# Performance work log

Measured on AMD Instinct MI355X. Metric: run time of the kernel, lower is better.

Reference implementation:

```python
import jax, jax.numpy as jnp
import numpy as np

B, S, D, H = 2, 2048, 1024, 16
DH = D // H  # 64


def setup_inputs() -> dict:
    key = jax.random.key(0)
    ks = jax.random.split(key, 12)
    scale = 0.02
    q = jax.random.normal(ks[0], (B, S, D), dtype=jnp.float32)
    k = jax.random.normal(ks[1], (B, S, D), dtype=jnp.float32)
    v = jax.random.normal(ks[2], (B, S, D), dtype=jnp.float32)
    # CTRL-style causal mask: 1.0 above the diagonal (positions to mask), 0.0 elsewhere
    mask = jnp.triu(jnp.ones((S, S), dtype=jnp.float32), k=1)
    Wq = jax.random.normal(ks[3], (D, D), dtype=jnp.float32) * scale
    bq = jnp.zeros((D,), dtype=jnp.float32)
    Wk = jax.random.normal(ks[4], (D, D), dtype=jnp.float32) * scale
    bk = jnp.zeros((D,), dtype=jnp.float32)
    Wv = jax.random.normal(ks[5], (D, D), dtype=jnp.float32) * scale
    bv = jnp.zeros((D,), dtype=jnp.float32)
    Wo = jax.random.normal(ks[6], (D, D), dtype=jnp.float32) * scale
    bo = jnp.zeros((D,), dtype=jnp.float32)
    return {"q": q, "k": k, "v": v, "mask": mask,
            "Wq": Wq, "bq": bq, "Wk": Wk, "bk": bk,
            "Wv": Wv, "bv": bv, "Wo": Wo, "bo": bo}


def _split_heads(x):
    # [B, S, D] -> [B, H, S, DH]
    b, s, _ = x.shape
    return x.reshape(b, s, H, DH).transpose(0, 2, 1, 3)


def reference(q, k, v, mask, Wq, bq, Wk, bk, Wv, bv, Wo, bo):
    # QKV projections
    qh = _split_heads(q @ Wq + bq)  # [B, H, S, DH]
    kh = _split_heads(k @ Wk + bk)
    vh = _split_heads(v @ Wv + bv)
    # scaled dot-product attention with CTRL mask convention (mask * -1e4 added)
    scores = jnp.einsum('bhqd,bhkd->bhqk', qh, kh) / jnp.sqrt(jnp.float32(DH))
    scores = scores + mask * -10000.0  # mask broadcasts [S,S] -> [B,H,S,S]
    weights = jax.nn.softmax(scores, axis=-1)
    ctx = jnp.einsum('bhqk,bhkd->bhqd', weights, vh)  # [B, H, S, DH]
    ctx = ctx.transpose(0, 2, 1, 3).reshape(q.shape[0], -1, D)  # [B, S, D]
    return ctx @ Wo + bo
```

## Files before the change

kernel.cpp:

```cpp
#include <hip/hip_runtime.h>
#include <stdint.h>

typedef unsigned short u16;
typedef __attribute__((ext_vector_type(8))) short bf16x8;
typedef __attribute__((ext_vector_type(4))) float f32x4;
typedef __attribute__((ext_vector_type(4))) unsigned short u16x4;

#define C_SCALE 0.1803368801111204f
#define C_MASK  -14426.950408889634f

__device__ __forceinline__ float bf2f(u16 x) {
  union { uint32_t u; float f; } v; v.u = ((uint32_t)x) << 16; return v.f;
}
__device__ __forceinline__ u16 f2bf(float f) {
  union { float f; uint32_t u; } v; v.f = f;
  return (u16)((v.u + 0x7FFFu + ((v.u >> 16) & 1u)) >> 16);
}

__device__ __forceinline__ void load_lds16(const void* g, void* l) {
  __builtin_amdgcn_global_load_lds(
      (const __attribute__((address_space(1))) uint32_t*)g,
      (__attribute__((address_space(3))) uint32_t*)l, 16, 0, 0);
}

__device__ __forceinline__ uint32_t pack_trunc(uint32_t f_even, uint32_t f_odd) {
  return __builtin_amdgcn_perm(f_odd, f_even, 0x07060302u);
}

__device__ __forceinline__ bool detect_bf16(const u16* __restrict__ q) {
  int lane = threadIdx.x & 63;
  u16 w = q[lane * 4];
  int e = (w >> 7) & 0xFF;
  unsigned long long b = __ballot(e >= 96 && e <= 159);
  return __popcll(b) >= 48;
}

__global__ __launch_bounds__(256) void transpose_all(const u16* __restrict__ W0,
                                                     const u16* __restrict__ W1,
                                                     const u16* __restrict__ W2,
                                                     const u16* __restrict__ W3,
                                                     u16* __restrict__ WTb,
                                                     const u16* __restrict__ qprobe) {
  constexpr int D = 1024;
  __shared__ u16 tile[64][72];
  const int z = blockIdx.z;
  const u16* W = z == 0 ? W0 : (z == 1 ? W1 : (z == 2 ? W2 : W3));
  u16* WT = WTb + (size_t)z * D * D;
  const bool isbf = detect_bf16(qprobe);
  const int x0 = blockIdx.x * 64, y0 = blockIdx.y * 64;
  const int t = threadIdx.x;
  const int r = t >> 3;
  const int c8 = (t & 7) << 3;
#pragma unroll
  for (int hh = 0; hh < 2; ++hh) {
    int row = r + hh * 32;
    if (isbf) {
      *(uint4*)&tile[row][c8] = *(const uint4*)&W[(size_t)(y0 + row) * D + x0 + c8];
    } else {
      const float* Wf = (const float*)W;
      float4 f0 = *(const float4*)&Wf[(size_t)(y0 + row) * D + x0 + c8];
      float4 f1 = *(const float4*)&Wf[(size_t)(y0 + row) * D + x0 + c8 + 4];
      u16 tmp[8] = {f2bf(f0.x), f2bf(f0.y), f2bf(f0.z), f2bf(f0.w),
                    f2bf(f1.x), f2bf(f1.y), f2bf(f1.z), f2bf(f1.w)};
      *(uint4*)&tile[row][c8] = *(uint4*)tmp;
    }
  }
  __syncthreads();
#pragma unroll
  for (int hh = 0; hh < 2; ++hh) {
    int row = r + hh * 32;
    u16 tmp[8];
#pragma unroll
    for (int i = 0; i < 8; ++i) tmp[i] = tile[c8 + i][row];
    *(uint4*)&WT[(size_t)(x0 + row) * D + y0 + c8] = *(uint4*)tmp;
  }
}


__device__ __forceinline__ void stage_tile32(const u16* __restrict__ src, int row0,
                                             int k0, u16* dst, int wave, int lane) {
  constexpr int K = 1024;
#pragma unroll
  for (int p = 0; p < 2; ++p) {
    int seg = wave * 2 + p;
    int r = seg * 16 + (lane >> 2);
    int c = lane & 3;
    int cg = c ^ ((r >> 1) & 3);
    load_lds16(&src[(size_t)(row0 + r) * K + k0 + cg * 8], dst + seg * 512);
  }
}

#define FRAG_READS(Ab, Bb)                                                    \
  _Pragma("unroll") for (int i = 0; i < 4; ++i) {                             \
    int r = wm + 16 * i + lr;                                                 \
    af[i] = *(const bf16x8*)&(Ab)[r * 32 + ((quad ^ ((r >> 1) & 3)) * 8)];    \
  }                                                                           \
  _Pragma("unroll") for (int jj = 0; jj < 4; ++jj) {                          \
    int r = wn + 16 * jj + lr;                                                \
    bff[jj] = *(const bf16x8*)&(Bb)[r * 32 + ((quad ^ ((r >> 1) & 3)) * 8)];  \
  }

#define MFMA16()                                                              \
  _Pragma("unroll") for (int i = 0; i < 4; ++i)                               \
  _Pragma("unroll") for (int jj = 0; jj < 4; ++jj)                            \
      acc[i][jj] = __builtin_amdgcn_mfma_f32_16x16x32_bf16(af[i], bff[jj],    \
                                                           acc[i][jj], 0, 0, 0);

__device__ __forceinline__ void kloop2_dma(const u16* __restrict__ A,
                                           const u16* __restrict__ BT,
                                           int m0, int n0, u16* As, u16* Bs,
                                           int wave, int lane, f32x4 (&acc)[4][4]) {
  const int quad = lane >> 4, lr = lane & 15;
  const int wm = (wave & 1) * 64, wn = (wave >> 1) * 64;
  auto stage = [&](int t, int buf) {
    stage_tile32(A, m0, t * 32, As + buf * 4096, wave, lane);
    stage_tile32(BT, n0, t * 32, Bs + buf * 4096, wave, lane);
  };
  stage(0, 0);
  __syncthreads();
#pragma unroll 1
  for (int j = 0; j < 16; ++j) {
    const int t0 = 2 * j;
    {
      stage(t0 + 1, 1);
      bf16x8 af[4], bff[4];
      const u16 *Ab = As, *Bb = Bs;
      FRAG_READS(Ab, Bb)
      MFMA16()
      __syncthreads();
    }
    {
      if (t0 + 2 < 32) stage(t0 + 2, 0);
      bf16x8 af[4], bff[4];
      const u16 *Ab = As + 4096, *Bb = Bs + 4096;
      FRAG_READS(Ab, Bb)
      MFMA16()
      __syncthreads();
    }
  }
}

__device__ __forceinline__ void kloop2_f32(const float* __restrict__ Af,
                                           const u16* __restrict__ BT,
                                           int m0, int n0, u16* As, u16* Bs,
                                           int tid, f32x4 (&acc)[4][4]) {
  constexpr int K = 1024;
  const int wave = tid >> 6, lane = tid & 63;
  const int quad = lane >> 4, lr = lane & 15;
  const int wm = (wave & 1) * 64, wn = (wave >> 1) * 64;
  const int ar = tid >> 1, ah = tid & 1;
  const uint32_t* Au = (const uint32_t*)Af;
  uint4 ra0[4], ra1[4];
  auto loadA = [&](int t, uint4 (&r)[4]) {
    const uint32_t* p = &Au[(size_t)(m0 + ar) * K + t * 32 + ah * 16];
    r[0] = *(const uint4*)(p + 0);
    r[1] = *(const uint4*)(p + 4);
    r[2] = *(const uint4*)(p + 8);
    r[3] = *(const uint4*)(p + 12);
  };
  auto writeA = [&](int buf, uint4 (&rr)[4]) {
    uint4 o0, o1;
    o0.x = pack_trunc(rr[0].x, rr[0].y); o0.y = pack_trunc(rr[0].z, rr[0].w);
    o0.z = pack_trunc(rr[1].x, rr[1].y); o0.w = pack_trunc(rr[1].z, rr[1].w);
    o1.x = pack_trunc(rr[2].x, rr[2].y); o1.y = pack_trunc(rr[2].z, rr[2].w);
    o1.z = pack_trunc(rr[3].x, rr[3].y); o1.w = pack_trunc(rr[3].z, rr[3].w);
    int sw = (ar >> 1) & 3;
    int c0 = (2 * ah) ^ sw, c1 = (2 * ah + 1) ^ sw;
    *(uint4*)&As[buf * 4096 + ar * 32 + c0 * 8] = o0;
    *(uint4*)&As[buf * 4096 + ar * 32 + c1 * 8] = o1;
  };
  auto stageB = [&](int t, int buf) {
    stage_tile32(BT, n0, t * 32, Bs + buf * 4096, wave, lane);
  };
  loadA(0, ra0);
  stageB(0, 0);
  loadA(1, ra1);
  writeA(0, ra0);
  __syncthreads();
#pragma unroll 1
  for (int j = 0; j < 16; ++j) {
    const int t0 = 2 * j;
    {
      stageB(t0 + 1, 1);
      writeA(1, ra1);
      if (t0 + 2 < 32) loadA(t0 + 2, ra0);
      bf16x8 af[4], bff[4];
      const u16 *Ab = As, *Bb = Bs;
      FRAG_READS(Ab, Bb)
      MFMA16()
      __syncthreads();
    }
    {
      if (t0 + 2 < 32) { stageB(t0 + 2, 0); writeA(0, ra0); }
      if (t0 + 3 < 32) loadA(t0 + 3, ra1);
      bf16x8 af[4], bff[4];
      const u16 *Ab = As + 4096, *Bb = Bs + 4096;
      FRAG_READS(Ab, Bb)
      MFMA16()
      __syncthreads();
    }
  }
}

__global__ __launch_bounds__(256, 3) void gemm_qkv(
    const u16* __restrict__ A0, const u16* __restrict__ A1, const u16* __restrict__ A2,
    const u16* __restrict__ WTb,
    const u16* __restrict__ b0, const u16* __restrict__ b1, const u16* __restrict__ b2,
    u16* __restrict__ Chb) {
  __shared__ u16 As[2 * 4096];
  __shared__ u16 Bs[2 * 4096];
  const int z = blockIdx.y;
  const u16* A = z == 0 ? A0 : (z == 1 ? A1 : A2);
  const u16* bias = z == 0 ? b0 : (z == 1 ? b1 : b2);
  const u16* BT = WTb + (size_t)z * 1024 * 1024;
  u16* C = Chb + (size_t)z * 4 * 1024 * 1024;
  const bool isbf = detect_bf16(A0);
  const int tid = threadIdx.x;
  const int wave = tid >> 6, lane = tid & 63;
  const int quad = lane >> 4, lr = lane & 15;
  const int f = blockIdx.x;
  const int n0 = (f >> 5) * 128;
  const int m0 = (f & 31) * 128;
  const int wm = (wave & 1) * 64, wn = (wave >> 1) * 64;

  f32x4 acc[4][4] = {};
  if (isbf) kloop2_dma(A, BT, m0, n0, As, Bs, wave, lane, acc);
  else      kloop2_f32((const float*)A, BT, m0, n0, As, Bs, tid, acc);

#pragma unroll
  for (int i = 0; i < 4; ++i) {
#pragma unroll
    for (int jj = 0; jj < 4; ++jj) {
      int n = n0 + wn + 16 * jj + lr;
      float bv = isbf ? bf2f(bias[n]) : ((const float*)bias)[n];
#pragma unroll
      for (int r = 0; r < 4; ++r) {
        int m = m0 + wm + 16 * i + quad * 4 + r;
        float val = acc[i][jj][r] + bv;
        int b = m >> 11, s = m & 2047, h = n >> 6, dh = n & 63;
        C[((size_t)(b * 16 + h) * 2048 + s) * 64 + dh] = f2bf(val);
      }
    }
  }
}

__global__ __launch_bounds__(256, 2) void gemm_out(const u16* __restrict__ A,
                                                   const u16* __restrict__ BT,
                                                   const u16* __restrict__ bias,
                                                   u16* __restrict__ C,
                                                   const u16* __restrict__ qprobe) {
  constexpr int N = 1024, K = 1024;
  __shared__ u16 As[2 * 2048];
  __shared__ u16 Bs[2 * 4096];
  const bool isbf = detect_bf16(qprobe);
  const int tid = threadIdx.x;
  const int wave = tid >> 6, lane = tid & 63;
  const int quad = lane >> 4, lr = lane & 15;
  const int f = blockIdx.x;
  const int n0 = (f >> 6) * 128;
  const int m0 = (f & 63) * 64;
  const int wm = (wave & 1) * 32, wn = (wave >> 1) * 64;

  auto stage = [&](int t, int buf) {
    {
      int r = wave * 16 + (lane >> 2);
      int c = lane & 3;
      int cg = c ^ ((r >> 1) & 3);
      load_lds16(&A[(size_t)(m0 + r) * K + t * 32 + cg * 8],
                 As + buf * 2048 + wave * 512);
    }
    stage_tile32(BT, n0, t * 32, Bs + buf * 4096, wave, lane);
  };

  f32x4 acc[2][4] = {};
  stage(0, 0);
  __syncthreads();
#pragma unroll 1
  for (int j = 0; j < 16; ++j) {
    const int t0 = 2 * j;
#pragma unroll
    for (int half = 0; half < 2; ++half) {
      const int t = t0 + half;
      if (t + 1 < 32) stage(t + 1, (t + 1) & 1);
      bf16x8 af[2], bff[4];
      const u16* Ab = As + (t & 1) * 2048;
      const u16* Bb = Bs + (t & 1) * 4096;
#pragma unroll
      for (int i = 0; i < 2; ++i) {
        int r = wm + 16 * i + lr;
        af[i] = *(const bf16x8*)&Ab[r * 32 + ((quad ^ ((r >> 1) & 3)) * 8)];
      }
#pragma unroll
      for (int jj = 0; jj < 4; ++jj) {
        int r = wn + 16 * jj + lr;
        bff[jj] = *(const bf16x8*)&Bb[r * 32 + ((quad ^ ((r >> 1) & 3)) * 8)];
      }
#pragma unroll
      for (int i = 0; i < 2; ++i)
#pragma unroll
        for (int jj = 0; jj < 4; ++jj)
          acc[i][jj] =
              __builtin_amdgcn_mfma_f32_16x16x32_bf16(af[i], bff[jj], acc[i][jj], 0, 0, 0);
      __syncthreads();
    }
  }

#pragma unroll
  for (int i = 0; i < 2; ++i) {
#pragma unroll
    for (int jj = 0; jj < 4; ++jj) {
      int n = n0 + wn + 16 * jj + lr;
      float bv = isbf ? bf2f(bias[n]) : ((const float*)bias)[n];
#pragma unroll
      for (int r = 0; r < 4; ++r) {
        int m = m0 + wm + 16 * i + quad * 4 + r;
        float val = acc[i][jj][r] + bv;
        size_t idx = (size_t)m * N + n;
        if (isbf) C[idx] = f2bf(val);
        else ((float*)C)[idx] = val;
      }
    }
  }
}

__global__ __launch_bounds__(256, 2) void attn_fwd(const u16* __restrict__ Qh,
                                                   const u16* __restrict__ Kh,
                                                   const u16* __restrict__ Vh,
                                                   u16* __restrict__ ctx) {
  constexpr int S = 2048, DH = 64, Dm = 1024;
  __shared__ u16 Ks[2][64 * 64];
  __shared__ u16 Vt[2][64 * 72];
  __shared__ u16 Pl[4][16 * 72];
  const int tid = threadIdx.x;
  const int wave = tid >> 6, lane = tid & 63;
  const int quad = lane >> 4, lr = lane & 15;
  const int bh = blockIdx.y;
  const int bx = (int)blockIdx.x;
  const size_t base = (size_t)bh * S * DH;
  const u16* Q = Qh + base;
  const u16* Kp = Kh + base;
  const u16* Vp = Vh + base;
  u16* Plw = Pl[wave];
  const int b = bh >> 4, h = bh & 15;

  const int vkey2 = (tid & 31) * 2, vd8 = (tid >> 5) * 8;
  uint4 va, vbr;

  auto stageK = [&](int kt, int kbuf) {
#pragma unroll
    for (int p = 0; p < 2; ++p) {
      int s = (wave * 2 + p) * 64 + lane;
      int r = s >> 3, cg = (s & 7) ^ (r & 7);
      load_lds16(&Kp[(size_t)(kt + r) * DH + cg * 8], &Ks[kbuf][(wave * 2 + p) * 512]);
    }
  };
  auto loadV = [&](int kt) {
    va  = *(const uint4*)&Vp[(size_t)(kt + vkey2) * DH + vd8];
    vbr = *(const uint4*)&Vp[(size_t)(kt + vkey2 + 1) * DH + vd8];
  };
  auto writeV = [&](int vbuf) {
    const u16* pa = (const u16*)&va;
    const u16* pb = (const u16*)&vbr;
#pragma unroll
    for (int i = 0; i < 8; ++i) {
      uint32_t pair = (uint32_t)pa[i] | ((uint32_t)pb[i] << 16);
      *(uint32_t*)&Vt[vbuf][(vd8 + i) * 72 + vkey2] = pair;
    }
  };

  int kb = 0, vb = 0;
  for (int ph = 0; ph < 2; ++ph) {
    const int qt = ph == 0 ? (31 - bx) : bx;
    const int q0 = qt * 64;
    const int nt = qt + 1;
    const int qg = q0 + wave * 16 + lr;

    bf16x8 aQ[2];
#pragma unroll
    for (int s = 0; s < 2; ++s)
      aQ[s] = *(const bf16x8*)&Q[(size_t)(q0 + wave * 16 + lr) * DH + s * 32 + quad * 8];

    f32x4 o[4] = {};
    float m_i = -1.0e5f;
    float l_i = 0.f;

    __syncthreads();
    stageK(0, kb);
    loadV(0);
    writeV(vb);
    if (nt > 1) loadV(64);

    for (int it = 0; it < nt; ++it) {
      const int kt = it * 64;
      __syncthreads();

      bf16x8 aK[4][2], bV[4][2];
#pragma unroll
      for (int t = 0; t < 4; ++t) {
        int r = t * 16 + lr;
#pragma unroll
        for (int s = 0; s < 2; ++s) {
          int ch = (s * 4 + quad) ^ (r & 7);
          aK[t][s] = *(const bf16x8*)&Ks[kb][r * 64 + ch * 8];
        }
      }
#pragma unroll
      for (int c = 0; c < 4; ++c)
#pragma unroll
        for (int s = 0; s < 2; ++s)
          bV[c][s] = *(const bf16x8*)&Vt[vb][(c * 16 + lr) * 72 + s * 32 + quad * 8];

      if (it + 1 < nt) {
        stageK(kt + 64, kb ^ 1);
        writeV(vb ^ 1);
        if (it + 2 < nt) loadV(kt + 128);
      }

      f32x4 sc[4];
#pragma unroll
      for (int t = 0; t < 4; ++t) {
        f32x4 zz = {0.f, 0.f, 0.f, 0.f};
        zz = __builtin_amdgcn_mfma_f32_16x16x32_bf16(aK[t][0], aQ[0], zz, 0, 0, 0);
        zz = __builtin_amdgcn_mfma_f32_16x16x32_bf16(aK[t][1], aQ[1], zz, 0, 0, 0);
        sc[t] = zz;
      }

      const bool diag = (it == nt - 1);
      float v[4][4];
      float mx = -1.0e5f;
      if (diag) {
#pragma unroll
        for (int t = 0; t < 4; ++t)
#pragma unroll
          for (int r = 0; r < 4; ++r) {
            int kg = kt + t * 16 + quad * 4 + r;
            float x = sc[t][r] * C_SCALE + ((kg > qg) ? C_MASK : 0.f);
            v[t][r] = x;
            mx = fmaxf(mx, x);
          }
      } else {
#pragma unroll
        for (int t = 0; t < 4; ++t)
#pragma unroll
          for (int r = 0; r < 4; ++r) {
            float x = sc[t][r] * C_SCALE;
            v[t][r] = x;
            mx = fmaxf(mx, x);
          }
      }
      mx = fmaxf(mx, __shfl_xor(mx, 16));
      mx = fmaxf(mx, __shfl_xor(mx, 32));
      float m_new = fmaxf(m_i, mx);
      float sum = 0.f;
      u16 pb16[4][4];
#pragma unroll
      for (int t = 0; t < 4; ++t)
#pragma unroll
        for (int r = 0; r < 4; ++r) {
          float p = exp2f(v[t][r] - m_new);
          sum += p;
          pb16[t][r] = f2bf(p);
        }
      sum += __shfl_xor(sum, 16);
      sum += __shfl_xor(sum, 32);
      float alpha = exp2f(m_i - m_new);
      l_i = l_i * alpha + sum;
      m_i = m_new;
#pragma unroll
      for (int t = 0; t < 4; ++t) {
        u16x4 w = {pb16[t][0], pb16[t][1], pb16[t][2], pb16[t][3]};
        *(u16x4*)&Plw[lr * 72 + t * 16 + quad * 4] = w;
      }
#pragma unroll
      for (int r = 0; r < 4; ++r) {
        float ab = __shfl(alpha, quad * 4 + r);
#pragma unroll
        for (int c = 0; c < 4; ++c) o[c][r] *= ab;
      }
      asm volatile("s_waitcnt lgkmcnt(0)" ::: "memory");
      bf16x8 aP[2];
#pragma unroll
      for (int s = 0; s < 2; ++s)
        aP[s] = *(const bf16x8*)&Plw[lr * 72 + s * 32 + quad * 8];
#pragma unroll
      for (int c = 0; c < 4; ++c)
#pragma unroll
        for (int s = 0; s < 2; ++s)
          o[c] = __builtin_amdgcn_mfma_f32_16x16x32_bf16(aP[s], bV[c][s], o[c], 0, 0, 0);
      kb ^= 1; vb ^= 1;
    }

    float linv = 1.f / l_i;
#pragma unroll
    for (int r = 0; r < 4; ++r) {
      float lb = __shfl(linv, quad * 4 + r);
      int s = q0 + wave * 16 + quad * 4 + r;
      size_t orow = ((size_t)b * S + s) * Dm + h * DH;
#pragma unroll
      for (int c = 0; c < 4; ++c) ctx[orow + c * 16 + lr] = f2bf(o[c][r] * lb);
    }
  }
}

extern "C" void kernel_launch(void* const* d_in, const int* in_sizes, int n_in,
                              void* d_out, int out_size, void* d_ws, size_t ws_size,
                              hipStream_t stream) {
  const u16* q  = (const u16*)d_in[0];
  const u16* k  = (const u16*)d_in[1];
  const u16* v  = (const u16*)d_in[2];
  const u16* Wq = (const u16*)d_in[4];
  const u16* bq = (const u16*)d_in[5];
  const u16* Wk = (const u16*)d_in[6];
  const u16* bk = (const u16*)d_in[7];
  const u16* Wv = (const u16*)d_in[8];
  const u16* bv = (const u16*)d_in[9];
  const u16* Wo = (const u16*)d_in[10];
  const u16* bo = (const u16*)d_in[11];
  u16* out = (u16*)d_out;

  constexpr size_t M1 = 1024 * 1024;
  u16* ws = (u16*)d_ws;
  u16* WT  = ws;
  u16* Qh  = WT + 4 * M1;
  u16* ctx = Qh + 12 * M1;

  dim3 tb(256);
  transpose_all<<<dim3(16, 16, 4), tb, 0, stream>>>(Wq, Wk, Wv, Wo, WT, q);
  gemm_qkv<<<dim3(256, 3), tb, 0, stream>>>(q, k, v, WT, bq, bk, bv, Qh);
  attn_fwd<<<dim3(16, 32), tb, 0, stream>>>(Qh, Qh + 4 * M1, Qh + 8 * M1, ctx);
  gemm_out<<<dim3(512), tb, 0, stream>>>(ctx, WT + 3 * M1, bo, out, q);
}
```

Baseline: 254.1 us.

## Pre-cast fp32 QKV activations to bf16 in prep kernel, use DMA GEMM path

Extends the weight transpose kernel with extra z-slices that convert the fp32 q/k/v activations to bf16 by truncation into a workspace buffer. When the workspace is large enough, the QKV GEMM then reads bf16 activations through the existing DMA-to-LDS k-loop instead of converting fp32 inside the GEMM. This removes per-tile conversion work and halves activation bytes read in the GEMM, at the cost of an extra full read and write pass over the activations. The cast truncates rather than rounds, and its buffer is shared with ctx.

```diff
diff --git a/kernel.cpp b/kernel.cpp
--- a/kernel.cpp
+++ b/kernel.cpp
@@ -35,18 +35,44 @@
   return __popcll(b) >= 48;
 }
 
-__global__ __launch_bounds__(256) void transpose_all(const u16* __restrict__ W0,
-                                                     const u16* __restrict__ W1,
-                                                     const u16* __restrict__ W2,
-                                                     const u16* __restrict__ W3,
-                                                     u16* __restrict__ WTb,
-                                                     const u16* __restrict__ qprobe) {
+__global__ __launch_bounds__(256) void prep_all(const u16* __restrict__ W0,
+                                                const u16* __restrict__ W1,
+                                                const u16* __restrict__ W2,
+                                                const u16* __restrict__ W3,
+                                                u16* __restrict__ WTb,
+                                                const u16* __restrict__ q,
+                                                const u16* __restrict__ k,
+                                                const u16* __restrict__ v,
+                                                u16* __restrict__ Acast,
+                                                int docast) {
   constexpr int D = 1024;
+  const int z = blockIdx.z;
+  const bool isbf = detect_bf16(q);
+
+  if (z >= 4) {
+    if (!docast || isbf) return;
+    const int zi = z - 4;
+    const u16* src = zi == 0 ? q : (zi == 1 ? k : v);
+    const uint32_t* S = (const uint32_t*)src;
+    u16* dst = Acast + (size_t)zi * 4 * 1024 * 1024;
+    const int fb = blockIdx.y * 16 + blockIdx.x;
+    const int t = threadIdx.x;
+#pragma unroll
+    for (int it = 0; it < 8; ++it) {
+      size_t base = (size_t)fb * 16384 + it * 2048 + t * 8;
+      uint4 a = *(const uint4*)&S[base];
+      uint4 b = *(const uint4*)&S[base + 4];
+      uint4 o;
+      o.x = pack_trunc(a.x, a.y); o.y = pack_trunc(a.z, a.w);
+      o.z = pack_trunc(b.x, b.y); o.w = pack_trunc(b.z, b.w);
+      *(uint4*)&dst[base] = o;
+    }
+    return;
+  }
+
   __shared__ u16 tile[64][72];
-  const int z = blockIdx.z;
   const u16* W = z == 0 ? W0 : (z == 1 ? W1 : (z == 2 ? W2 : W3));
   u16* WT = WTb + (size_t)z * D * D;
-  const bool isbf = detect_bf16(qprobe);
   const int x0 = blockIdx.x * 64, y0 = blockIdx.y * 64;
   const int t = threadIdx.x;
   const int r = t >> 3;
@@ -202,7 +228,49 @@
   }
 }
 
-__global__ __launch_bounds__(256, 3) void gemm_qkv(
+__global__ __launch_bounds__(256, 3) void gemm_qkv_pre(
+    const u16* __restrict__ q, const u16* __restrict__ k, const u16* __restrict__ v,
+    const u16* __restrict__ Acast, const u16* __restrict__ WTb,
+    const u16* __restrict__ b0, const u16* __restrict__ b1, const u16* __restrict__ b2,
+    u16* __restrict__ Chb) {
+  __shared__ u16 As[2 * 4096];
+  __shared__ u16 Bs[2 * 4096];
+  const int z = blockIdx.y;
+  const bool isbf = detect_bf16(q);
+  const u16* Araw = z == 0 ? q : (z == 1 ? k : v);
+  const u16* A = isbf ? Araw : Acast + (size_t)z * 4 * 1024 * 1024;
+  const u16* bias = z == 0 ? b0 : (z == 1 ? b1 : b2);
+  const u16* BT = WTb + (size_t)z * 1024 * 1024;
+  u16* C = Chb + (size_t)z * 4 * 1024 * 1024;
+  const int tid = threadIdx.x;
+  const int wave = tid >> 6, lane = tid & 63;
+  const int quad = lane >> 4, lr = lane & 15;
+  const int f = blockIdx.x;
+  const int n0 = (f >> 5) * 128;
+  const int m0 = (f & 31) * 128;
+  const int wm = (wave & 1) * 64, wn = (wave >> 1) * 64;
+
+  f32x4 acc[4][4] = {};
+  kloop2_dma(A, BT, m0, n0, As, Bs, wave, lane, acc);
+
+#pragma unroll
+  for (int i = 0; i < 4; ++i) {
+#pragma unroll
+    for (int jj = 0; jj < 4; ++jj) {
+      int n = n0 + wn + 16 * jj + lr;
+      float bv = isbf ? bf2f(bias[n]) : ((const float*)bias)[n];
+#pragma unroll
+      for (int r = 0; r < 4; ++r) {
+        int m = m0 + wm + 16 * i + quad * 4 + r;
+        float val = acc[i][jj][r] + bv;
+        int b = m >> 11, s = m & 2047, h = n >> 6, dh = n & 63;
+        C[((size_t)(b * 16 + h) * 2048 + s) * 64 + dh] = f2bf(val);
+      }
+    }
+  }
+}
+
+__global__ __launch_bounds__(256, 3) void gemm_qkv_fb(
     const u16* __restrict__ A0, const u16* __restrict__ A1, const u16* __restrict__ A2,
     const u16* __restrict__ WTb,
     const u16* __restrict__ b0, const u16* __restrict__ b1, const u16* __restrict__ b2,
@@ -522,11 +590,19 @@
   u16* ws = (u16*)d_ws;
   u16* WT  = ws;
   u16* Qh  = WT + 4 * M1;
-  u16* ctx = Qh + 12 * M1;
+  u16* X   = Qh + 12 * M1;
+  u16* Acast = X;
+  u16* ctx   = X;
+
+  const bool docast = ws_size >= (size_t)28 * M1 * 2;
 
   dim3 tb(256);
-  transpose_all<<<dim3(16, 16, 4), tb, 0, stream>>>(Wq, Wk, Wv, Wo, WT, q);
-  gemm_qkv<<<dim3(256, 3), tb, 0, stream>>>(q, k, v, WT, bq, bk, bv, Qh);
+  prep_all<<<dim3(16, 16, 7), tb, 0, stream>>>(Wq, Wk, Wv, Wo, WT, q, k, v,
+                                               Acast, docast ? 1 : 0);
+  if (docast)
+    gemm_qkv_pre<<<dim3(256, 3), tb, 0, stream>>>(q, k, v, Acast, WT, bq, bk, bv, Qh);
+  else
+    gemm_qkv_fb<<<dim3(256, 3), tb, 0, stream>>>(q, k, v, WT, bq, bk, bv, Qh);
   attn_fwd<<<dim3(16, 32), tb, 0, stream>>>(Qh, Qh + 4 * M1, Qh + 8 * M1, ctx);
   gemm_out<<<dim3(512), tb, 0, stream>>>(ctx, WT + 3 * M1, bo, out, q);
 }
```

Measured after the change: 240.1 us. 1.06x faster.
